# Performance work log

Measured on AMD Instinct MI355X. Metric: run time of the kernel, lower is better.

## Reference

```python
import jax, jax.numpy as jnp
import numpy as np


def setup_inputs() -> dict:
    key = jax.random.key(0)
    ks = jax.random.split(key, 7)
    B, P, D = 32, 576, 768   # batch, tokens (24x24 patches), inp_dim
    H, HD = 12, 64           # n_heads, head_dim = inp_dim // n_heads
    s = 0.02
    return {
        "x": jax.random.normal(ks[0], (B, P, D), dtype=jnp.float32),
        "Wq": jax.random.normal(ks[1], (H, D, HD), dtype=jnp.float32) * s,
        "bq": jax.random.normal(ks[2], (H, HD), dtype=jnp.float32) * s,
        "Wk": jax.random.normal(ks[3], (H, D, HD), dtype=jnp.float32) * s,
        "bk": jax.random.normal(ks[4], (H, HD), dtype=jnp.float32) * s,
        "Wv": jax.random.normal(ks[5], (H, D, HD), dtype=jnp.float32) * s,
        "bv": jax.random.normal(ks[6], (H, HD), dtype=jnp.float32) * s,
    }


def reference(x, Wq, bq, Wk, bk, Wv, bv):
    # Per-head independent linear projections (stacked over head axis h).
    # x: [b, p, d]; Wq/Wk/Wv: [h, d, k]; biases: [h, k]
    q = jnp.einsum("bpd,hdk->bhpk", x, Wq) + bq[None, :, None, :]
    k = jnp.einsum("bpd,hdk->bhpk", x, Wk) + bk[None, :, None, :]
    v = jnp.einsum("bpd,hdk->bhpk", x, Wv) + bv[None, :, None, :]
    head_dim = k.shape[-1]
    scale = 1.0 / jnp.sqrt(jnp.asarray(head_dim, dtype=x.dtype))
    attn = jnp.einsum("bhqk,bhpk->bhqp", q, k) * scale  # [b, h, p, p]
    attn = jax.nn.softmax(attn, axis=-1)
    out = jnp.einsum("bhqp,bhpk->bhqk", attn, v)        # [b, h, p, k]
    b, h, p, hd = out.shape
    # concat heads along last dim (dropout is identity in eval mode)
    return jnp.transpose(out, (0, 2, 1, 3)).reshape(b, p, h * hd)
```

## Files before the change

kernel.cpp:

```cpp
#include <hip/hip_runtime.h>
#include <hip/hip_bf16.h>

typedef unsigned short ushort_t;
typedef unsigned int u32;
typedef float f32x4 __attribute__((ext_vector_type(4)));
typedef short short8 __attribute__((ext_vector_type(8)));

#define WT_BYTES  (36*64*768*2)
#define KV_BYTES  (32*12*576*64*2)
#define QSCALE    0.18033688f

static __device__ __forceinline__ ushort_t f2bf(float f) {
    return __builtin_bit_cast(ushort_t, (__bf16)f);
}
static __device__ __forceinline__ short8 pack8(float4 a, float4 b) {
    union { ushort_t u[8]; short8 v; } pk;
    pk.u[0]=f2bf(a.x); pk.u[1]=f2bf(a.y); pk.u[2]=f2bf(a.z); pk.u[3]=f2bf(a.w);
    pk.u[4]=f2bf(b.x); pk.u[5]=f2bf(b.y); pk.u[6]=f2bf(b.z); pk.u[7]=f2bf(b.w);
    return pk.v;
}
static __device__ __forceinline__ u32 pkbf(float a, float b) {
    union { __hip_bfloat162 h; u32 u; } c;
    c.h = __float22bfloat162_rn(float2{a, b});
    return c.u;
}
static __device__ __forceinline__ void gl_lds16(const ushort_t* g, ushort_t* l) {
    __builtin_amdgcn_global_load_lds((const __attribute__((address_space(1))) u32*)g,
                                     (__attribute__((address_space(3))) u32*)l, 16, 0, 0);
}
static __device__ __forceinline__ int swzb(int row, int chunk) {
    return row * 128 + (((chunk ^ (row & 7)) & 7) << 4);
}
#define MFMA16 __builtin_amdgcn_mfma_f32_16x16x32_bf16

__global__ __launch_bounds__(256) void prep(
    const float* __restrict__ Wq, const float* __restrict__ Wk,
    const float* __restrict__ Wv, const float* __restrict__ x,
    ushort_t* __restrict__ Wt, ushort_t* __restrict__ xb)
{
    int idx = blockIdx.x * 256 + threadIdx.x;
    if (idx < 221184) {
        int d0   = (idx % 96) * 8;
        int rest = idx / 96;
        int hd   = rest & 63;
        int ph   = rest >> 6;
        int h    = ph % 12, pr = ph / 12;
        const float* W = (pr == 0) ? Wq : (pr == 1 ? Wk : Wv);
        union { ushort_t u[8]; short8 v; } pk;
        #pragma unroll
        for (int j = 0; j < 8; ++j)
            pk.u[j] = f2bf(W[(size_t)(h * 768 + d0 + j) * 64 + hd]);
        *(short8*)(Wt + ((size_t)(ph * 64 + hd)) * 768 + d0) = pk.v;
    } else {
        size_t e = (size_t)(idx - 221184) * 8;
        const float4* xp = (const float4*)(x + e);
        *(short8*)(xb + e) = pack8(xp[0], xp[1]);
    }
}

__global__ __launch_bounds__(256) void proj_kv(
    const ushort_t* __restrict__ xb, const ushort_t* __restrict__ Wt,
    const float* __restrict__ bq, const float* __restrict__ bk,
    const float* __restrict__ bv,
    ushort_t* __restrict__ Qb, ushort_t* __restrict__ Kb,
    ushort_t* __restrict__ Vtb, int nts, int ph_base)
{
    __shared__ ushort_t smem[18432];

    const int t = threadIdx.x;
    const int w = t >> 6, l = t & 63, m16 = l & 15, g = l >> 4;
    const int wm = w >> 1, wn = w & 1;

    int L = blockIdx.y * gridDim.x + blockIdx.x;
    int xcd = L & 7, jj_ = L >> 3;
    int nt = jj_ % nts, mt = (jj_ / nts) * 8 + xcd;
    const int m0 = mt * 128;
    const int ph0 = ph_base + nt * 2;

    const int grow = l >> 3, gch = (l & 7) ^ grow;

    auto stageA = [&](int kc) {
        #pragma unroll
        for (int c4 = 0; c4 < 4; ++c4) {
            int ci = w * 4 + c4;
            gl_lds16(xb + (size_t)(m0 + ci * 8 + grow) * 768 + kc * 64 + gch * 8,
                     smem + ci * 512);
        }
    };
    auto stageB = [&](int kc) {
        #pragma unroll
        for (int c4 = 0; c4 < 4; ++c4) {
            int ci = w * 4 + c4;
            int r  = ci * 8 + grow;
            gl_lds16(Wt + ((size_t)(ph0 + (r >> 6)) * 64 + (r & 63)) * 768 + kc * 64 + gch * 8,
                     smem + 8192 + ci * 512);
        }
    };

    f32x4 acc[4][4] = {};

    for (int kc = 0; kc < 12; ++kc) {
        __syncthreads();
        stageA(kc); stageB(kc);
        __syncthreads();
        __builtin_amdgcn_s_setprio(1);
        #pragma unroll
        for (int jj = 0; jj < 2; ++jj) {
            short8 af[4], bf[4];
            #pragma unroll
            for (int mi = 0; mi < 4; ++mi)
                af[mi] = *(const short8*)((char*)smem + swzb(wm * 64 + mi * 16 + m16, jj * 4 + g));
            #pragma unroll
            for (int ni = 0; ni < 4; ++ni)
                bf[ni] = *(const short8*)((char*)smem + 16384 + swzb(wn * 64 + ni * 16 + m16, jj * 4 + g));
            #pragma unroll
            for (int mi = 0; mi < 4; ++mi)
                #pragma unroll
                for (int ni = 0; ni < 4; ++ni)
                    acc[mi][ni] = MFMA16(af[mi], bf[ni], acc[mi][ni], 0, 0, 0);
        }
        __builtin_amdgcn_s_setprio(0);
    }
    __syncthreads();

    const int ph = ph0 + wn, proj = ph / 12, h = ph % 12;
    const float* bias = (proj == 0 ? bq : (proj == 1 ? bk : bv)) + h * 64;
    const float qs = (proj == 0) ? QSCALE : 1.0f;
    const int tokg0 = m0 + wm * 64;
    const int bb = tokg0 / 576, pp = tokg0 % 576;
    ushort_t* sE = smem + w * 4608;

    #pragma unroll
    for (int ni = 0; ni < 4; ++ni) {
        float bvv = bias[ni * 16 + m16];
        #pragma unroll
        for (int mi = 0; mi < 4; ++mi)
            #pragma unroll
            for (int i = 0; i < 4; ++i) {
                float val = (acc[mi][ni][i] + bvv) * qs;
                int tok = mi * 16 + g * 4 + i;
                int hd  = ni * 16 + m16;
                if (proj < 2) sE[tok * 72 + hd] = f2bf(val);
                else          sE[hd * 72 + tok] = f2bf(val);
            }
    }
    if (proj < 2) {
        ushort_t* dst = (proj == 0 ? Qb : Kb) + ((size_t)(bb * 12 + h) * 576 + pp) * 64;
        #pragma unroll
        for (int rr = 0; rr < 8; ++rr) {
            int row = rr * 8 + (l >> 3), ch = l & 7;
            *(short8*)(dst + (size_t)row * 64 + ch * 8) = *(const short8*)&sE[row * 72 + ch * 8];
        }
    } else {
        ushort_t* dst = Vtb + (size_t)(bb * 12 + h) * 64 * 576 + pp;
        #pragma unroll
        for (int rr = 0; rr < 8; ++rr) {
            int hd = rr * 8 + (l >> 3), tc = l & 7;
            *(short8*)(dst + (size_t)hd * 576 + tc * 8) = *(const short8*)&sE[hd * 72 + tc * 8];
        }
    }
}

__global__ __launch_bounds__(256) void proj_reg(
    const float* __restrict__ x, const ushort_t* __restrict__ Wt,
    const float* __restrict__ bk, const float* __restrict__ bv,
    ushort_t* __restrict__ Kb, ushort_t* __restrict__ Vtb)
{
    __shared__ ushort_t smem[22528];

    const int t = threadIdx.x;
    const int w = t >> 6, l = t & 63, m16 = l & 15, g = l >> 4;
    const int wm = w >> 1, wn = w & 1;

    int L = blockIdx.y * 12 + blockIdx.x;
    int xcd = L & 7, jj_ = L >> 3;
    int nt = jj_ % 12, mt = (jj_ / 12) * 8 + xcd;
    const int m0 = mt * 96;
    const int b  = mt / 6, pb = (mt % 6) * 96;

    const int grow = l >> 3, gch = (l & 7) ^ grow;

    float4 ar[3][2];
    auto loadA = [&](int kc) {
        #pragma unroll
        for (int q = 0; q < 3; ++q) {
            int c = t + q * 256, row = c >> 3, ch = c & 7;
            const float4* xp = (const float4*)(x + (size_t)(m0 + row) * 768 + kc * 64 + ch * 8);
            ar[q][0] = xp[0]; ar[q][1] = xp[1];
        }
    };
    auto writeA = [&]() {
        #pragma unroll
        for (int q = 0; q < 3; ++q) {
            int c = t + q * 256, row = c >> 3, ch = c & 7;
            *(short8*)((char*)smem + swzb(row, ch)) = pack8(ar[q][0], ar[q][1]);
        }
    };
    auto stageB = [&](int kc, int d) {
        #pragma unroll
        for (int c4 = 0; c4 < 4; ++c4) {
            int ci = w * 4 + c4;
            const ushort_t* gs = Wt + (size_t)((12 + nt * 2) * 64 + ci * 8 + grow) * 768
                               + kc * 64 + gch * 8;
            gl_lds16(gs, smem + 6144 + d * 8192 + ci * 512);
        }
    };

    f32x4 acc[3][4] = {};
    loadA(0); stageB(0, 0); writeA();
    __syncthreads();

    for (int kc = 0; kc < 12; ++kc) {
        const int d = kc & 1;
        if (kc < 11) { loadA(kc + 1); stageB(kc + 1, d ^ 1); }
        __builtin_amdgcn_s_setprio(1);
        #pragma unroll
        for (int jj = 0; jj < 2; ++jj) {
            short8 af[3], bf[4];
            #pragma unroll
            for (int mi = 0; mi < 3; ++mi)
                af[mi] = *(const short8*)((char*)smem + swzb(wm * 48 + mi * 16 + m16, jj * 4 + g));
            #pragma unroll
            for (int ni = 0; ni < 4; ++ni)
                bf[ni] = *(const short8*)((char*)smem + 12288 + d * 16384 + swzb(wn * 64 + ni * 16 + m16, jj * 4 + g));
            #pragma unroll
            for (int mi = 0; mi < 3; ++mi)
                #pragma unroll
                for (int ni = 0; ni < 4; ++ni)
                    acc[mi][ni] = MFMA16(af[mi], bf[ni], acc[mi][ni], 0, 0, 0);
        }
        __builtin_amdgcn_s_setprio(0);
        __syncthreads();
        if (kc < 11) { writeA(); __syncthreads(); }
    }

    const int ph = 12 + nt * 2 + wn;
    const int proj = ph / 12, h = ph % 12;
    const float* bias = (proj == 1 ? bk : bv) + h * 64;
    ushort_t* sE = smem + w * 4608;

    #pragma unroll
    for (int ni = 0; ni < 4; ++ni) {
        float bvv = bias[ni * 16 + m16];
        #pragma unroll
        for (int mi = 0; mi < 3; ++mi)
            #pragma unroll
            for (int i = 0; i < 4; ++i) {
                float val = acc[mi][ni][i] + bvv;
                int tok = mi * 16 + g * 4 + i;
                int hd  = ni * 16 + m16;
                if (proj == 1) sE[tok * 72 + hd] = f2bf(val);
                else           sE[hd * 72 + tok] = f2bf(val);
            }
    }
    if (proj == 1) {
        ushort_t* dst = Kb + ((size_t)(b * 12 + h) * 576 + pb + wm * 48) * 64;
        #pragma unroll
        for (int rr = 0; rr < 6; ++rr) {
            int row = rr * 8 + (l >> 3), ch = l & 7;
            *(short8*)(dst + (size_t)row * 64 + ch * 8) = *(const short8*)&sE[row * 72 + ch * 8];
        }
    } else {
        ushort_t* dst = Vtb + (size_t)(b * 12 + h) * 64 * 576 + pb + wm * 48;
        #pragma unroll
        for (int rr = 0; rr < 8; ++rr) {
            int hd = rr * 8 + (l >> 3), tc = l & 7;
            if (tc < 6)
                *(short8*)(dst + (size_t)hd * 576 + tc * 8) = *(const short8*)&sE[hd * 72 + tc * 8];
        }
    }
}

template<int MODE>
__global__ __launch_bounds__(256) void attn_k(
    const float* __restrict__ x, const ushort_t* __restrict__ xb,
    const ushort_t* __restrict__ Wt, const float* __restrict__ bq,
    const ushort_t* __restrict__ Qb, const ushort_t* __restrict__ Kb,
    const ushort_t* __restrict__ Vtb, float* __restrict__ out)
{
    __shared__ ushort_t smem[20480];

    const int t = threadIdx.x;
    const int w = t >> 6, l = t & 63, m16 = l & 15, g = l >> 4;

    int L = blockIdx.y * 9 + blockIdx.x;
    int xcd = L & 7, jj_ = L >> 3;
    int qt = jj_ % 9, bh = (jj_ / 9) * 8 + xcd;
    const int b = bh / 12, h = bh % 12;
    const int p0 = qt * 64;

    const int grow = l >> 3, gch = (l & 7) ^ grow;
    const int spbase = 32768 + w * 2048;

    short8 aq0, aq1;

    if constexpr (MODE == 3) {
        const ushort_t* qsrc = Qb + ((size_t)bh * 576 + p0 + w * 16 + m16) * 64 + g * 8;
        aq0 = *(const short8*)qsrc;
        aq1 = *(const short8*)(qsrc + 32);
    } else {
        f32x4 acc[4] = {};
        auto stage = [&](int kc, int d) {
            const int boff = d ? 24576 : 16384;
            if constexpr (MODE == 2) {
                #pragma unroll
                for (int c2 = 0; c2 < 2; ++c2) {
                    int ci = w * 2 + c2;
                    gl_lds16(xb + (size_t)(b * 576 + p0 + ci * 8 + grow) * 768 + kc * 64 + gch * 8,
                             smem + (d * 8192 + ci * 1024) / 2);
                    gl_lds16(Wt + (size_t)(h * 64 + ci * 8 + grow) * 768 + kc * 64 + gch * 8,
                             smem + (boff + ci * 1024) / 2);
                }
            } else {
                const int row = t >> 2, c16 = (t & 3) * 16;
                const float4* xp = (const float4*)(x + (size_t)(b * 576 + p0 + row) * 768 + kc * 64 + c16);
                float4 u0 = xp[0], u1 = xp[1], u2 = xp[2], u3 = xp[3];
                *(short8*)((char*)smem + d * 8192 + swzb(row, c16 >> 3))       = pack8(u0, u1);
                *(short8*)((char*)smem + d * 8192 + swzb(row, (c16 >> 3) + 1)) = pack8(u2, u3);
                #pragma unroll
                for (int c2 = 0; c2 < 2; ++c2) {
                    int ci = w * 2 + c2;
                    gl_lds16(Wt + (size_t)(h * 64 + ci * 8 + grow) * 768 + kc * 64 + gch * 8,
                             smem + (boff + ci * 1024) / 2);
                }
            }
        };
        stage(0, 0); __syncthreads();
        for (int kc = 0; kc < 12; ++kc) {
            int d = kc & 1;
            const int boff = d ? 24576 : 16384;
            if (kc < 11) stage(kc + 1, d ^ 1);
            __builtin_amdgcn_s_setprio(1);
            #pragma unroll
            for (int jj = 0; jj < 2; ++jj) {
                short8 a = *(const short8*)((char*)smem + d * 8192 + swzb(w * 16 + m16, jj * 4 + g));
                #pragma unroll
                for (int f = 0; f < 4; ++f) {
                    short8 bb = *(const short8*)((char*)smem + boff + swzb(f * 16 + m16, jj * 4 + g));
                    acc[f] = MFMA16(a, bb, acc[f], 0, 0, 0);
                }
            }
            __builtin_amdgcn_s_setprio(0);
            __syncthreads();
        }
        #pragma unroll
        for (int f = 0; f < 4; ++f) {
            float bqv = bq[h * 64 + f * 16 + m16];
            #pragma unroll
            for (int i = 0; i < 4; ++i) {
                float val = (acc[f][i] + bqv) * QSCALE;
                int r = g * 4 + i, c = f * 16 + m16;
                *(ushort_t*)((char*)smem + spbase + r * 128
                    + (((((c >> 3) ^ (r & 7)) & 7) << 4) | ((c & 7) << 1))) = f2bf(val);
            }
        }
        aq0 = *(const short8*)((char*)smem + spbase + m16 * 128 + (((g ^ (m16 & 7)) & 7) << 4));
        aq1 = *(const short8*)((char*)smem + spbase + m16 * 128 + ((((4 + g) ^ (m16 & 7)) & 7) << 4));
        __syncthreads();
    }

    const ushort_t* Kbase = Kb  + (size_t)bh * (576 * 64);
    const ushort_t* Vbase = Vtb + (size_t)bh * (64 * 576);

    auto stageK = [&](int kt, int d) {
        #pragma unroll
        for (int c2 = 0; c2 < 2; ++c2) {
            int ci = w * 2 + c2;
            gl_lds16(Kbase + (size_t)(kt * 64 + ci * 8 + grow) * 64 + gch * 8,
                     smem + (d * 8192 + ci * 1024) / 2);
        }
    };
    auto stageV = [&](int kt, int d) {
        #pragma unroll
        for (int c2 = 0; c2 < 2; ++c2) {
            int ci = w * 2 + c2;
            gl_lds16(Vbase + (size_t)(ci * 8 + grow) * 576 + kt * 64 + gch * 8,
                     smem + (16384 + d * 8192 + ci * 1024) / 2);
        }
    };

    char* const spw  = (char*)smem + spbase + m16 * 128 + (g & 1) * 8;
    char* const spr0 = (char*)smem + spbase + m16 * 128 + (((g     ) ^ (m16 & 7)) << 4);
    char* const spr1 = (char*)smem + spbase + m16 * 128 + (((4 + g) ^ (m16 & 7)) << 4);

    f32x4 psumv = {};
    f32x4 accO[4] = {};

    stageK(0, 0); stageV(0, 0);
    __syncthreads();
    for (int kt = 0; kt < 9; ++kt) {
        int d = kt & 1;
        if (kt < 8) { stageV(kt + 1, d ^ 1); stageK(kt + 1, d ^ 1); }

        f32x4 s[4] = {};
        __builtin_amdgcn_s_setprio(1);
        #pragma unroll
        for (int jj = 0; jj < 2; ++jj) {
            short8 qf = jj ? aq1 : aq0;
            #pragma unroll
            for (int f = 0; f < 4; ++f) {
                short8 kf = *(const short8*)((char*)smem + d * 8192 + swzb(f * 16 + m16, jj * 4 + g));
                s[f] = MFMA16(kf, qf, s[f], 0, 0, 0);
            }
        }
        __builtin_amdgcn_s_setprio(0);

        #pragma unroll
        for (int f = 0; f < 4; ++f) {
            #pragma unroll
            for (int i = 0; i < 4; ++i)
                s[f][i] = exp2f(s[f][i]);
            psumv += s[f];
        }

        #pragma unroll
        for (int f = 0; f < 4; ++f) {
            uint2 pkd = { pkbf(s[f][0], s[f][1]), pkbf(s[f][2], s[f][3]) };
            int ch = ((2 * f + (g >> 1)) ^ (m16 & 7)) << 4;
            *(uint2*)(spw + ch) = pkd;
        }
        short8 pa0 = *(const short8*)spr0;
        short8 pa1 = *(const short8*)spr1;

        __builtin_amdgcn_s_setprio(1);
        #pragma unroll
        for (int jj = 0; jj < 2; ++jj) {
            short8 paj = jj ? pa1 : pa0;
            #pragma unroll
            for (int f = 0; f < 4; ++f) {
                short8 bv_ = *(const short8*)((char*)smem + 16384 + d * 8192 + swzb(f * 16 + m16, jj * 4 + g));
                accO[f] = MFMA16(paj, bv_, accO[f], 0, 0, 0);
            }
        }
        __builtin_amdgcn_s_setprio(0);
        __syncthreads();
    }

    float ps = psumv[0] + psumv[1] + psumv[2] + psumv[3];
    ps += __shfl_xor(ps, 16, 64);
    ps += __shfl_xor(ps, 32, 64);
    float invq = 1.0f / ps;
    float inv[4];
    #pragma unroll
    for (int i = 0; i < 4; ++i)
        inv[i] = __shfl(invq, g * 4 + i, 64);

    float* orow = out + ((size_t)b * 576 + p0 + w * 16) * 768 + h * 64;
    #pragma unroll
    for (int f = 0; f < 4; ++f)
        #pragma unroll
        for (int i = 0; i < 4; ++i)
            orow[(size_t)(g * 4 + i) * 768 + f * 16 + m16] = accO[f][i] * inv[i];
}

extern "C" void kernel_launch(void* const* d_in, const int* in_sizes, int n_in,
                              void* d_out, int out_size, void* d_ws, size_t ws_size,
                              hipStream_t stream) {
    const float* x  = (const float*)d_in[0];
    const float* Wq = (const float*)d_in[1];
    const float* bq = (const float*)d_in[2];
    const float* Wk = (const float*)d_in[3];
    const float* bk = (const float*)d_in[4];
    const float* Wv = (const float*)d_in[5];
    const float* bv = (const float*)d_in[6];
    float* out = (float*)d_out;

    const size_t T3 = (size_t)WT_BYTES + 4 * (size_t)KV_BYTES;
    const size_t T2 = (size_t)WT_BYTES + 3 * (size_t)KV_BYTES;

    if (ws_size >= T3) {
        ushort_t* Wt  = (ushort_t*)d_ws;
        ushort_t* xbp = (ushort_t*)((char*)d_ws + WT_BYTES);
        ushort_t* Qb  = (ushort_t*)((char*)d_ws + WT_BYTES + (size_t)KV_BYTES);
        ushort_t* Kb  = (ushort_t*)((char*)d_ws + WT_BYTES + 2 * (size_t)KV_BYTES);
        ushort_t* Vtb = (ushort_t*)((char*)d_ws + WT_BYTES + 3 * (size_t)KV_BYTES);
        hipLaunchKernelGGL(prep, dim3(7776), dim3(256), 0, stream, Wq, Wk, Wv, x, Wt, xbp);
        hipLaunchKernelGGL(proj_kv, dim3(18, 144), dim3(256), 0, stream,
                           xbp, Wt, bq, bk, bv, Qb, Kb, Vtb, 18, 0);
        hipLaunchKernelGGL((attn_k<3>), dim3(9, 384), dim3(256), 0, stream,
                           x, xbp, Wt, bq, Qb, Kb, Vtb, out);
    } else if (ws_size >= T2) {
        ushort_t* Wt  = (ushort_t*)d_ws;
        ushort_t* xbp = (ushort_t*)((char*)d_ws + WT_BYTES);
        ushort_t* Kb  = (ushort_t*)((char*)d_ws + WT_BYTES + (size_t)KV_BYTES);
        ushort_t* Vtb = (ushort_t*)((char*)d_ws + WT_BYTES + 2 * (size_t)KV_BYTES);
        hipLaunchKernelGGL(prep, dim3(7776), dim3(256), 0, stream, Wq, Wk, Wv, x, Wt, xbp);
        hipLaunchKernelGGL(proj_kv, dim3(12, 144), dim3(256), 0, stream,
                           xbp, Wt, bq, bk, bv, (ushort_t*)nullptr, Kb, Vtb, 12, 12);
        hipLaunchKernelGGL((attn_k<2>), dim3(9, 384), dim3(256), 0, stream,
                           x, xbp, Wt, bq, (const ushort_t*)nullptr, Kb, Vtb, out);
    } else {
        ushort_t* Wt  = (ushort_t*)d_ws;
        ushort_t* Kb  = (ushort_t*)((char*)d_ws + WT_BYTES);
        ushort_t* Vtb = (ushort_t*)((char*)d_ws + WT_BYTES + (size_t)KV_BYTES);
        hipLaunchKernelGGL(prep, dim3(864), dim3(256), 0, stream, Wq, Wk, Wv, x, Wt, (ushort_t*)nullptr);
        hipLaunchKernelGGL(proj_reg, dim3(12, 192), dim3(256), 0, stream,
                           x, Wt, bk, bv, Kb, Vtb);
        hipLaunchKernelGGL((attn_k<1>), dim3(9, 384), dim3(256), 0, stream,
                           x, (const ushort_t*)nullptr, Wt, bq, (const ushort_t*)nullptr, Kb, Vtb, out);
    }
}
```

Baseline: 176.7 us.

## Use 144-row query tiles with 9-wave attention blocks and LDS-transposed weight prep

Adds attn9, an attention kernel where each 576-thread block handles 144 query rows with 9 waves. Each K/V tile staged into LDS is now shared by more queries, so K/V global traffic and block count drop roughly by 2.25x. Separately, the weight-transpose prep now reads coalesced float4 rows and transposes through shared memory instead of doing strided scalar loads. The cost is larger blocks with higher LDS use, which may lower occupancy, and only 8 of the 9 waves issue the staging loads.

```diff
diff --git a/kernel.cpp b/kernel.cpp
--- a/kernel.cpp
+++ b/kernel.cpp
@@ -38,21 +38,32 @@
     const float* __restrict__ Wv, const float* __restrict__ x,
     ushort_t* __restrict__ Wt, ushort_t* __restrict__ xb)
 {
-    int idx = blockIdx.x * 256 + threadIdx.x;
-    if (idx < 221184) {
-        int d0   = (idx % 96) * 8;
-        int rest = idx / 96;
-        int hd   = rest & 63;
-        int ph   = rest >> 6;
-        int h    = ph % 12, pr = ph / 12;
+    __shared__ ushort_t sT[64][136];
+    const int t = threadIdx.x;
+    if (blockIdx.x < 216) {
+        const int ph = blockIdx.x / 6, d0 = (blockIdx.x % 6) * 128;
+        const int h = ph % 12, pr = ph / 12;
         const float* W = (pr == 0) ? Wq : (pr == 1 ? Wk : Wv);
-        union { ushort_t u[8]; short8 v; } pk;
-        #pragma unroll
-        for (int j = 0; j < 8; ++j)
-            pk.u[j] = f2bf(W[(size_t)(h * 768 + d0 + j) * 64 + hd]);
-        *(short8*)(Wt + ((size_t)(ph * 64 + hd)) * 768 + d0) = pk.v;
+        #pragma unroll
+        for (int q = 0; q < 8; ++q) {
+            int e = q * 256 + t;
+            int d = e >> 4, c4 = (e & 15) * 4;
+            float4 v = *(const float4*)&W[(size_t)(h * 768 + d0 + d) * 64 + c4];
+            sT[c4 + 0][d] = f2bf(v.x);
+            sT[c4 + 1][d] = f2bf(v.y);
+            sT[c4 + 2][d] = f2bf(v.z);
+            sT[c4 + 3][d] = f2bf(v.w);
+        }
+        __syncthreads();
+        #pragma unroll
+        for (int q = 0; q < 4; ++q) {
+            int c = q * 256 + t;
+            int hd = c >> 4, ch = c & 15;
+            *(short8*)(Wt + (size_t)(ph * 64 + hd) * 768 + d0 + ch * 8) =
+                *(const short8*)&sT[hd][ch * 8];
+        }
     } else {
-        size_t e = (size_t)(idx - 221184) * 8;
+        size_t e = ((size_t)(blockIdx.x - 216) * 256 + t) * 8;
         const float4* xp = (const float4*)(x + e);
         *(short8*)(xb + e) = pack8(xp[0], xp[1]);
     }
@@ -271,12 +282,122 @@
     }
 }
 
+__global__ __launch_bounds__(576) void attn9(
+    const ushort_t* __restrict__ Qb, const ushort_t* __restrict__ Kb,
+    const ushort_t* __restrict__ Vtb, float* __restrict__ out)
+{
+    __shared__ ushort_t smem[25600];
+
+    const int t = threadIdx.x;
+    const int w = t >> 6, l = t & 63, m16 = l & 15, g = l >> 4;
+
+    int L = blockIdx.y * 4 + blockIdx.x;
+    int xcd = L & 7, jj_ = L >> 3;
+    int qt = jj_ % 4, bh = (jj_ / 4) * 8 + xcd;
+    const int b = bh / 12, h = bh % 12;
+    const int p0 = qt * 144;
+
+    const int grow = l >> 3, gch = (l & 7) ^ grow;
+    const int spbase = 32768 + w * 2048;
+
+    const ushort_t* qsrc = Qb + ((size_t)bh * 576 + p0 + w * 16 + m16) * 64 + g * 8;
+    short8 aq0 = *(const short8*)qsrc;
+    short8 aq1 = *(const short8*)(qsrc + 32);
+
+    const ushort_t* Kbase = Kb  + (size_t)bh * (576 * 64);
+    const ushort_t* Vbase = Vtb + (size_t)bh * (64 * 576);
+
+    auto stageK = [&](int kt, int d) {
+        if (w < 8)
+            gl_lds16(Kbase + (size_t)(kt * 64 + w * 8 + grow) * 64 + gch * 8,
+                     smem + (d * 8192 + w * 1024) / 2);
+    };
+    auto stageV = [&](int kt, int d) {
+        if (w < 8)
+            gl_lds16(Vbase + (size_t)(w * 8 + grow) * 576 + kt * 64 + gch * 8,
+                     smem + (16384 + d * 8192 + w * 1024) / 2);
+    };
+
+    char* const spw  = (char*)smem + spbase + m16 * 128 + (g & 1) * 8;
+    char* const spr0 = (char*)smem + spbase + m16 * 128 + (((g     ) ^ (m16 & 7)) << 4);
+    char* const spr1 = (char*)smem + spbase + m16 * 128 + (((4 + g) ^ (m16 & 7)) << 4);
+
+    f32x4 psumv = {};
+    f32x4 accO[4] = {};
+
+    stageK(0, 0); stageV(0, 0);
+    __syncthreads();
+    for (int kt = 0; kt < 9; ++kt) {
+        int d = kt & 1;
+        if (kt < 8) { stageV(kt + 1, d ^ 1); stageK(kt + 1, d ^ 1); }
+
+        f32x4 s[4] = {};
+        __builtin_amdgcn_s_setprio(1);
+        #pragma unroll
+        for (int jj = 0; jj < 2; ++jj) {
+            short8 qf = jj ? aq1 : aq0;
+            #pragma unroll
+            for (int f = 0; f < 4; ++f) {
+                short8 kf = *(const short8*)((char*)smem + d * 8192 + swzb(f * 16 + m16, jj * 4 + g));
+                s[f] = MFMA16(kf, qf, s[f], 0, 0, 0);
+            }
+        }
+        __builtin_amdgcn_s_setprio(0);
+
+        #pragma unroll
+        for (int f = 0; f < 4; ++f) {
+            #pragma unroll
+            for (int i = 0; i < 4; ++i)
+                s[f][i] = exp2f(s[f][i]);
+            psumv += s[f];
+        }
+
+        #pragma unroll
+        for (int f = 0; f < 4; ++f) {
+            uint2 pkd = { pkbf(s[f][0], s[f][1]), pkbf(s[f][2], s[f][3]) };
+            int ch = ((2 * f + (g >> 1)) ^ (m16 & 7)) << 4;
+            *(uint2*)(spw + ch) = pkd;
+        }
+        short8 pa0 = *(const short8*)spr0;
+        short8 pa1 = *(const short8*)spr1;
+
+        __builtin_amdgcn_s_setprio(1);
+        #pragma unroll
+        for (int jj = 0; jj < 2; ++jj) {
+            short8 paj = jj ? pa1 : pa0;
+            #pragma unroll
+            for (int f = 0; f < 4; ++f) {
+                short8 bv_ = *(const short8*)((char*)smem + 16384 + d * 8192 + swzb(f * 16 + m16, jj * 4 + g));
+                accO[f] = MFMA16(paj, bv_, accO[f], 0, 0, 0);
+            }
+        }
+        __builtin_amdgcn_s_setprio(0);
+        __syncthreads();
+    }
+
+    float ps = psumv[0] + psumv[1] + psumv[2] + psumv[3];
+    ps += __shfl_xor(ps, 16, 64);
+    ps += __shfl_xor(ps, 32, 64);
+    float invq = 1.0f / ps;
+    float inv[4];
+    #pragma unroll
+    for (int i = 0; i < 4; ++i)
+        inv[i] = __shfl(invq, g * 4 + i, 64);
+
+    float* orow = out + ((size_t)b * 576 + p0 + w * 16) * 768 + h * 64;
+    #pragma unroll
+    for (int f = 0; f < 4; ++f)
+        #pragma unroll
+        for (int i = 0; i < 4; ++i)
+            orow[(size_t)(g * 4 + i) * 768 + f * 16 + m16] = accO[f][i] * inv[i];
+}
+
 template<int MODE>
 __global__ __launch_bounds__(256) void attn_k(
     const float* __restrict__ x, const ushort_t* __restrict__ xb,
     const ushort_t* __restrict__ Wt, const float* __restrict__ bq,
-    const ushort_t* __restrict__ Qb, const ushort_t* __restrict__ Kb,
-    const ushort_t* __restrict__ Vtb, float* __restrict__ out)
+    const ushort_t* __restrict__ Kb, const ushort_t* __restrict__ Vtb,
+    float* __restrict__ out)
 {
     __shared__ ushort_t smem[20480];
 
@@ -293,12 +414,7 @@
     const int spbase = 32768 + w * 2048;
 
     short8 aq0, aq1;
-
-    if constexpr (MODE == 3) {
-        const ushort_t* qsrc = Qb + ((size_t)bh * 576 + p0 + w * 16 + m16) * 64 + g * 8;
-        aq0 = *(const short8*)qsrc;
-        aq1 = *(const short8*)(qsrc + 32);
-    } else {
+    {
         f32x4 acc[4] = {};
         auto stage = [&](int kc, int d) {
             const int boff = d ? 24576 : 16384;
@@ -474,29 +590,29 @@
         ushort_t* Qb  = (ushort_t*)((char*)d_ws + WT_BYTES + (size_t)KV_BYTES);
         ushort_t* Kb  = (ushort_t*)((char*)d_ws + WT_BYTES + 2 * (size_t)KV_BYTES);
         ushort_t* Vtb = (ushort_t*)((char*)d_ws + WT_BYTES + 3 * (size_t)KV_BYTES);
-        hipLaunchKernelGGL(prep, dim3(7776), dim3(256), 0, stream, Wq, Wk, Wv, x, Wt, xbp);
+        hipLaunchKernelGGL(prep, dim3(7128), dim3(256), 0, stream, Wq, Wk, Wv, x, Wt, xbp);
         hipLaunchKernelGGL(proj_kv, dim3(18, 144), dim3(256), 0, stream,
                            xbp, Wt, bq, bk, bv, Qb, Kb, Vtb, 18, 0);
-        hipLaunchKernelGGL((attn_k<3>), dim3(9, 384), dim3(256), 0, stream,
-                           x, xbp, Wt, bq, Qb, Kb, Vtb, out);
+        hipLaunchKernelGGL(attn9, dim3(4, 384), dim3(576), 0, stream,
+                           Qb, Kb, Vtb, out);
     } else if (ws_size >= T2) {
         ushort_t* Wt  = (ushort_t*)d_ws;
         ushort_t* xbp = (ushort_t*)((char*)d_ws + WT_BYTES);
         ushort_t* Kb  = (ushort_t*)((char*)d_ws + WT_BYTES + (size_t)KV_BYTES);
         ushort_t* Vtb = (ushort_t*)((char*)d_ws + WT_BYTES + 2 * (size_t)KV_BYTES);
-        hipLaunchKernelGGL(prep, dim3(7776), dim3(256), 0, stream, Wq, Wk, Wv, x, Wt, xbp);
+        hipLaunchKernelGGL(prep, dim3(7128), dim3(256), 0, stream, Wq, Wk, Wv, x, Wt, xbp);
         hipLaunchKernelGGL(proj_kv, dim3(12, 144), dim3(256), 0, stream,
                            xbp, Wt, bq, bk, bv, (ushort_t*)nullptr, Kb, Vtb, 12, 12);
         hipLaunchKernelGGL((attn_k<2>), dim3(9, 384), dim3(256), 0, stream,
-                           x, xbp, Wt, bq, (const ushort_t*)nullptr, Kb, Vtb, out);
+                           x, xbp, Wt, bq, Kb, Vtb, out);
     } else {
         ushort_t* Wt  = (ushort_t*)d_ws;
         ushort_t* Kb  = (ushort_t*)((char*)d_ws + WT_BYTES);
         ushort_t* Vtb = (ushort_t*)((char*)d_ws + WT_BYTES + (size_t)KV_BYTES);
-        hipLaunchKernelGGL(prep, dim3(864), dim3(256), 0, stream, Wq, Wk, Wv, x, Wt, (ushort_t*)nullptr);
+        hipLaunchKernelGGL(prep, dim3(216), dim3(256), 0, stream, Wq, Wk, Wv, x, Wt, (ushort_t*)nullptr);
         hipLaunchKernelGGL(proj_reg, dim3(12, 192), dim3(256), 0, stream,
                            x, Wt, bk, bv, Kb, Vtb);
         hipLaunchKernelGGL((attn_k<1>), dim3(9, 384), dim3(256), 0, stream,
-                           x, (const ushort_t*)nullptr, Wt, bq, (const ushort_t*)nullptr, Kb, Vtb, out);
-    }
-}
+                           x, (const ushort_t*)nullptr, Wt, bq, Kb, Vtb, out);
+    }
+}
```

New measurement: 180.0 us. About the same (+1.9%).
